# Performance work log

Hardware: AMD Instinct MI355X
Metric: run time of the kernel (lower is better)

The kernel has to match this reference:

```python
import jax, jax.numpy as jnp
import numpy as np

COMMITMENT_COST = 0.25


def setup_inputs() -> dict:
    key = jax.random.key(0)
    k1, k2 = jax.random.split(key)
    z = jax.random.normal(k1, (32, 256, 32, 32), dtype=jnp.float32)
    # Embedding init mirrors uniform(-1/codebook_size, 1/codebook_size)
    emb = jax.random.uniform(k2, (4096, 256), dtype=jnp.float32,
                             minval=-1.0 / 4096, maxval=1.0 / 4096)
    return {"z": z, "emb": emb}


def reference(z, emb):
    # z: [b, c, h, w] with c == token_size; emb: [codebook_size, token_size]
    b, c, h, w = z.shape
    z_bhwc = jnp.transpose(z, (0, 2, 3, 1))           # [b, h, w, c]
    z_flat = z_bhwc.reshape(-1, c)                    # [N, c]

    # Squared-distance matrix: ||z||^2 + ||e||^2 - 2 z e^T  -> [N, K]
    d = (jnp.sum(z_flat * z_flat, axis=1, keepdims=True)
         + jnp.sum(emb * emb, axis=1)
         - 2.0 * jnp.einsum('nd,kd->nk', z_flat, emb))

    idx = jnp.argmin(d, axis=1)                       # [N]
    z_q = emb[idx].reshape(z_bhwc.shape)              # [b, h, w, c]

    commitment_loss = COMMITMENT_COST * jnp.mean(
        (jax.lax.stop_gradient(z_q) - z_bhwc) ** 2)
    codebook_loss = jnp.mean((z_q - jax.lax.stop_gradient(z_bhwc)) ** 2)
    loss = commitment_loss + codebook_loss

    # Straight-through estimator
    z_q = z_bhwc + jax.lax.stop_gradient(z_q - z_bhwc)
    z_q = jnp.transpose(z_q, (0, 3, 1, 2))            # [b, c, h, w]

    min_encoding_indices = idx.reshape(b, h, w)
    return z_q, loss, commitment_loss, codebook_loss, min_encoding_indices
```

## Files before the change

### kernel.cpp

```cpp
#include <hip/hip_runtime.h>

#define CDIM 256
#define CB   4096
#define HW   1024
#define NTOK 32768
#define NELEM 8388608
#define MARGIN 3.5e-4f
#define OVCAP 64

typedef float f32x4 __attribute__((ext_vector_type(4)));
typedef short bf16x8 __attribute__((ext_vector_type(8)));
typedef unsigned int u32;
typedef unsigned long long u64;

__device__ __forceinline__ unsigned short f2bf(float x) {
    u32 b = __float_as_uint(x);
    return (unsigned short)((b + 0x7fffu + ((b >> 16) & 1u)) >> 16);
}
__device__ __forceinline__ u32 fenc(float f) {
    u32 b = __float_as_uint(f);
    return (b & 0x80000000u) ? ~b : (b | 0x80000000u);
}
__device__ __forceinline__ float fdec(u32 u) {
    return __uint_as_float((u & 0x80000000u) ? (u & 0x7fffffffu) : ~u);
}
__device__ __forceinline__ u64 shfl_xor_u64(u64 v, int s) {
    u32 lo = __shfl_xor((u32)v, s);
    u32 hi = __shfl_xor((u32)(v >> 32), s);
    return ((u64)hi << 32) | lo;
}
__device__ __forceinline__ void gl_lds16(const void* g, void* l) {
    __builtin_amdgcn_global_load_lds(
        (const __attribute__((address_space(1))) u32*)g,
        (__attribute__((address_space(3))) u32*)l, 16, 0, 0);
}


__global__ __launch_bounds__(1024) void prep(const float* __restrict__ z,
                                             const float* __restrict__ emb,
                                             float* __restrict__ zT,
                                             unsigned short* __restrict__ z_hip,
                                             float* __restrict__ zn,
                                             u32* __restrict__ ovcnt,
                                             float* __restrict__ enorm2,
                                             unsigned short* __restrict__ e_hip,
                                             u32* __restrict__ cnt2) {
    __shared__ float T[128][64];
    const int tid = threadIdx.x;
    const int tg = blockIdx.x;
    if (tid < 16) {
        const int code = tg * 8 + (tid >> 1);
        const int cl = code & 127;
        const int cgE = code >> 7;
        const int sxzE = (cl >> 1) & 3;
        float s = 0.f;
#pragma unroll
        for (int kb = 0; kb < 4; ++kb) {
            const int c0 = (tid & 1) * 128 + kb * 32;
            const int kc = c0 >> 5;
            __align__(16) unsigned short tmp[32];
#pragma unroll
            for (int q = 0; q < 8; ++q) {
                float4 v = *(const float4*)(emb + (size_t)code * CDIM + c0 + 4 * q);
                s += v.x * v.x + v.y * v.y + v.z * v.z + v.w * v.w;
                tmp[4 * q + 0] = f2bf(v.x); tmp[4 * q + 1] = f2bf(v.y);
                tmp[4 * q + 2] = f2bf(v.z); tmp[4 * q + 3] = f2bf(v.w);
            }
            uint4* dst4 = (uint4*)(e_hip + (((size_t)(cgE * 8 + kc) * 128 + cl) * 32));
#pragma unroll
            for (int q = 0; q < 4; ++q)
                dst4[q ^ sxzE] = *(uint4*)&tmp[8 * q];
        }
        s += __shfl_xor(s, 1);
        if ((tid & 1) == 0) enorm2[code] = s;
        if (tg == 0 && tid == 0) *cnt2 = 0u;
    }
    const int b = tg >> 4, hw0 = (tg * 64) & 1023;
    const float* zb = z + (size_t)b * (CDIM * HW) + hw0;
    const int tt = tid & 63;
    const int qrole = tid >> 6;
    const int kcl = qrole >> 2;
    const int qq = qrole & 3;
    const int gz = tg >> 1;
    const int rowl = (tg & 1) * 64 + tt;
    const int sxz = (tt >> 1) & 3;
    float zacc = 0.f;
#pragma unroll
    for (int grp = 0; grp < 2; ++grp) {
        const int c0 = grp * 128;
        __syncthreads();
#pragma unroll
        for (int p = 0; p < 8; ++p) {
            const int c = p * 16 + qrole;
            T[c][tt] = zb[(size_t)(c0 + c) * HW + tt];
        }
        __syncthreads();
        const int kc = grp * 4 + kcl;
        const int cb = kcl * 32 + qq * 8;
        float* dstT = zT + (size_t)(tg * 64 + tt) * CDIM + c0 + cb;
        __align__(16) unsigned short us[8];
#pragma unroll
        for (int q = 0; q < 2; ++q) {
            float4 v;
            v.x = T[cb + 4 * q + 0][tt]; v.y = T[cb + 4 * q + 1][tt];
            v.z = T[cb + 4 * q + 2][tt]; v.w = T[cb + 4 * q + 3][tt];
            ((float4*)dstT)[q] = v;
            zacc += v.x * v.x + v.y * v.y + v.z * v.z + v.w * v.w;
            us[4 * q + 0] = f2bf(v.x); us[4 * q + 1] = f2bf(v.y);
            us[4 * q + 2] = f2bf(v.z); us[4 * q + 3] = f2bf(v.w);
        }
        uint4* d4 = (uint4*)(z_hip + (((size_t)(gz * 8 + kc) * 128 + rowl) * 32));
        d4[qq ^ sxz] = *(uint4*)&us[0];
    }
    __syncthreads();
    float* zp = &T[0][0];
    zp[qrole * 64 + tt] = zacc;
    __syncthreads();
    if (tid < 64) {
        float s = 0.f;
#pragma unroll
        for (int r = 0; r < 16; ++r) s += zp[r * 64 + tid];
        zn[tg * 64 + tid] = s;
        ovcnt[tg * 64 + tid] = 0u;
    }
}


__global__ __launch_bounds__(256, 4) void p1(const unsigned short* __restrict__ z_hip,
                                             const unsigned short* __restrict__ e_hip,
                                             const float* __restrict__ enorm2,
                                             u64* __restrict__ cand,
                                             u32* __restrict__ ovcnt,
                                             u64* __restrict__ ovslot) {
    __shared__ __align__(16) unsigned short Bs[2][128 * 32];
    const int bid = blockIdx.x;
    const int xcd = bid & 7;
    const int seq = bid >> 3;
    const int rg = xcd * 32 + (seq >> 5);
    const int cg = seq & 31;
    const int tid = threadIdx.x;
    const int w = tid >> 6, lane = tid & 63;
    const int quad = lane >> 4, l15 = lane & 15;
    const int swz = (quad ^ ((l15 >> 1) & 3)) * 8;

    f32x4 acc[2][8];
#pragma unroll
    for (int i = 0; i < 2; ++i)
#pragma unroll
        for (int j = 0; j < 8; ++j)
#pragma unroll
            for (int e = 0; e < 4; ++e) acc[i][j][e] = 0.f;

    const char* gB = (const char*)e_hip + ((size_t)cg << 16) + w * 2048 + lane * 16;
    const char* gA0 = (const char*)z_hip + ((size_t)rg << 16)
                      + (w * 32 + l15) * 64 + swz * 2;
    char* lB = (char*)Bs + w * 2048;
    gl_lds16(gB, lB);           gl_lds16(gB + 1024, lB + 1024);
    gB += 8192;
    bf16x8 af0 = *(const bf16x8*)(gA0);
    bf16x8 af1 = *(const bf16x8*)(gA0 + 1024);
    __syncthreads();
#pragma unroll
    for (int kc = 0; kc < 8; ++kc) {
        const int cur = kc & 1;
        bf16x8 afn0, afn1;
        if (kc < 7) {
            char* dB = lB + (cur ^ 1) * 8192;
            gl_lds16(gB, dB);       gl_lds16(gB + 1024, dB + 1024);
            gB += 8192;
            asm volatile("" ::: "memory");
            const char* gA = gA0 + (size_t)(kc + 1) * 8192;
            afn0 = *(const bf16x8*)(gA);
            afn1 = *(const bf16x8*)(gA + 1024);
        }
        const unsigned short* B0 = Bs[cur];
        __builtin_amdgcn_s_setprio(1);
#pragma unroll
        for (int nh = 0; nh < 2; ++nh) {
            bf16x8 bfr[4];
#pragma unroll
            for (int nj = 0; nj < 4; ++nj)
                bfr[nj] = *(const bf16x8*)&B0[((nh * 4 + nj) * 16 + l15) * 32 + swz];
#pragma unroll
            for (int nj = 0; nj < 4; ++nj) {
                acc[0][nh * 4 + nj] = __builtin_amdgcn_mfma_f32_16x16x32_bf16(
                    af0, bfr[nj], acc[0][nh * 4 + nj], 0, 0, 0);
                acc[1][nh * 4 + nj] = __builtin_amdgcn_mfma_f32_16x16x32_bf16(
                    af1, bfr[nj], acc[1][nh * 4 + nj], 0, 0, 0);
            }
        }
        __builtin_amdgcn_s_setprio(0);
        if (kc < 7) {
            af0 = afn0; af1 = afn1;
            asm volatile("s_waitcnt vmcnt(2)" ::: "memory");
            __builtin_amdgcn_s_barrier();
            asm volatile("" ::: "memory");
        }
    }
    float en[8];
#pragma unroll
    for (int ni = 0; ni < 8; ++ni) en[ni] = enorm2[cg * 128 + ni * 16 + l15];
#pragma unroll
    for (int mi = 0; mi < 2; ++mi) {
#pragma unroll
        for (int r = 0; r < 4; ++r) {
            const int row = w * 32 + mi * 16 + quad * 4 + r;
            const int t = rg * 128 + row;
            float dv[8];
#pragma unroll
            for (int ni = 0; ni < 8; ++ni) dv[ni] = en[ni] - 2.0f * acc[mi][ni][r];
            float m = fminf(fminf(fminf(dv[0], dv[1]), fminf(dv[2], dv[3])),
                            fminf(fminf(dv[4], dv[5]), fminf(dv[6], dv[7])));
            m = fminf(m, __shfl_xor(m, 1));
            m = fminf(m, __shfl_xor(m, 2));
            m = fminf(m, __shfl_xor(m, 4));
            m = fminf(m, __shfl_xor(m, 8));
            u32 myni = 8u;
#pragma unroll
            for (int ni = 7; ni >= 0; --ni)
                if (dv[ni] == m) myni = (u32)ni;
            const unsigned long long bal = __ballot(myni < 8u);
            const int sl = __ffs((u32)((bal >> (quad << 4)) & 0xFFFFu)) - 1;
            if (l15 == sl) {
                const u32 k = (u32)(cg * 128 + (int)myni * 16 + l15);
                cand[((size_t)t << 5) + cg] = ((u64)fenc(m) << 32) | k;
            }
            const float thr = m + MARGIN;
#pragma unroll
            for (int ni = 0; ni < 8; ++ni) {
                if (dv[ni] <= thr && !(l15 == sl && ni == (int)myni)) {
                    const u32 k = (u32)(cg * 128 + ni * 16 + l15);
                    const u32 pos = atomicAdd(&ovcnt[t], 1u);
                    if (pos < (u32)OVCAP)
                        ovslot[(size_t)t * OVCAP + pos] = ((u64)fenc(dv[ni]) << 32) | k;
                }
            }
        }
    }
}

__global__ __launch_bounds__(256) void k5(const float* __restrict__ zT,
                                          const float* __restrict__ emb,
                                          const float* __restrict__ enorm2,
                                          const float* __restrict__ zn,
                                          const u64* __restrict__ cand,
                                          const u32* __restrict__ ovcnt,
                                          const u64* __restrict__ ovslot,
                                          float* __restrict__ idxf,
                                          float* __restrict__ dmin) {
    const int t = (blockIdx.x * 256 + threadIdx.x) >> 6;
    const int lane = threadIdx.x & 63;
    const u64 pkv = cand[((size_t)t << 5) + (lane & 31)];
    u64 g = pkv;
#pragma unroll
    for (int s = 1; s < 32; s <<= 1) {
        const u64 o = shfl_xor_u64(g, s);
        g = o < g ? o : g;
    }
    const float thr = fdec((u32)(g >> 32)) + MARGIN;
    const float4 za = ((const float4*)(zT + (size_t)t * CDIM))[lane];
    const float znv = zn[t];
    float bdv = 1e30f; int bk = 0x7fffffff;
    unsigned long long q = __ballot(fdec((u32)(pkv >> 32)) <= thr)
                           & 0xFFFFFFFFull;
    while (q) {
        const int i = __ffsll(q) - 1; q &= q - 1;
        const int k = __shfl((int)(u32)pkv, i);
        const float4 ea = ((const float4*)(emb + (size_t)k * CDIM))[lane];
        float p = za.x * ea.x + za.y * ea.y + za.z * ea.z + za.w * ea.w;
#pragma unroll
        for (int s = 1; s < 64; s <<= 1) p += __shfl_xor(p, s);
        const float t1 = znv + enorm2[k];
        const float d = t1 - 2.0f * p;
        if (d < bdv || (d == bdv && k < bk)) { bdv = d; bk = k; }
    }
    u32 n = ovcnt[t]; if (n > (u32)OVCAP) n = (u32)OVCAP;
    for (u32 i = 0; i < n; ++i) {
        const u64 ov = ovslot[(size_t)t * OVCAP + i];
        if (!(fdec((u32)(ov >> 32)) <= thr)) continue;
        const int k = (int)(u32)ov;
        const float4 ea = ((const float4*)(emb + (size_t)k * CDIM))[lane];
        float p = za.x * ea.x + za.y * ea.y + za.z * ea.z + za.w * ea.w;
#pragma unroll
        for (int s = 1; s < 64; s <<= 1) p += __shfl_xor(p, s);
        const float t1 = znv + enorm2[k];
        const float d = t1 - 2.0f * p;
        if (d < bdv || (d == bdv && k < bk)) { bdv = d; bk = k; }
    }
    if (lane == 0) {
        idxf[t] = (float)bk;
        dmin[t] = bdv;
    }
}

__global__ __launch_bounds__(1024) void k2(const float* __restrict__ emb,
                                           const float* __restrict__ idxf,
                                           const float* __restrict__ dmin,
                                           float* __restrict__ zq,
                                           float* __restrict__ out3,
                                           u32* __restrict__ cnt2) {
    __shared__ int ks[64];
    __shared__ float red[1024];
    __shared__ int lastFlag;
    const int tid = threadIdx.x;
    const int tok0 = blockIdx.x * 64;
    const int b = tok0 >> 10, hw0 = tok0 & 1023;
    if (tid < 64) ks[tid] = (int)idxf[tok0 + tid];
    __syncthreads();
    const int t4 = (tid & 15) * 4;
    const int ka = ks[t4], kb = ks[t4 + 1], kc = ks[t4 + 2], kd = ks[t4 + 3];
    float* outb = zq + (size_t)b * (CDIM * HW) + hw0 + t4;
    int c = tid >> 4;
#pragma unroll
    for (int p = 0; p < 4; ++p, c += 64) {
        float4 v;
        v.x = emb[(size_t)ka * CDIM + c];
        v.y = emb[(size_t)kb * CDIM + c];
        v.z = emb[(size_t)kc * CDIM + c];
        v.w = emb[(size_t)kd * CDIM + c];
        *(float4*)(outb + (size_t)c * HW) = v;
    }
    if (tid == 0) lastFlag = (atomicAdd(cnt2, 1u) == 511u) ? 1 : 0;
    __syncthreads();
    if (lastFlag) {
        const float4* d4 = (const float4*)dmin;
        float s = 0.f;
        for (int i = tid; i < NTOK / 4; i += 1024) {
            const float4 v = d4[i];
            s += (v.x + v.y) + (v.z + v.w);
        }
        red[tid] = s;
        __syncthreads();
        for (int o = 512; o > 0; o >>= 1) {
            if (tid < o) red[tid] += red[tid + o];
            __syncthreads();
        }
        if (tid == 0) {
            const float mse = red[0] / (float)NELEM;
            out3[0] = 1.25f * mse;
            out3[1] = 0.25f * mse;
            out3[2] = mse;
        }
    }
}

extern "C" void kernel_launch(void* const* d_in, const int* in_sizes, int n_in,
                              void* d_out, int out_size, void* d_ws, size_t ws_size,
                              hipStream_t stream) {
    const float* z   = (const float*)d_in[0];
    const float* emb = (const float*)d_in[1];
    float* out = (float*)d_out;
    char* w = (char*)d_ws;

    float* zn     = (float*)w;                       w += NTOK * 4;
    float* enorm2 = (float*)w;                       w += CB * 4;
    u32*   ovcnt  = (u32*)w;                         w += NTOK * 4;
    float* dmin   = (float*)w;                       w += NTOK * 4;
    u32*   cnt2   = (u32*)w;                         w += 256;
    float* zT     = (float*)w;                       w += (size_t)NTOK * CDIM * 4;
    unsigned short* z_hip = (unsigned short*)w;      w += (size_t)NTOK * CDIM * 2;
    unsigned short* e_hip = (unsigned short*)w;      w += (size_t)CB * CDIM * 2;
    u64*   cand   = (u64*)w;                         w += (size_t)NTOK * 32 * 8;
    u64*   ovslot = (u64*)w;                         w += (size_t)NTOK * OVCAP * 8;
    float* idxf = out + NELEM + 3;

    hipLaunchKernelGGL(prep, dim3(512),       dim3(1024), 0, stream,
                       z, emb, zT, z_hip, zn, ovcnt, enorm2, e_hip, cnt2);
    hipLaunchKernelGGL(p1,  dim3((NTOK / 128) * (CB / 128)), dim3(256), 0, stream,
                       z_hip, e_hip, enorm2, cand, ovcnt, ovslot);
    hipLaunchKernelGGL(k5,  dim3(NTOK / 4),   dim3(256), 0, stream,
                       zT, emb, enorm2, zn, cand, ovcnt, ovslot, idxf, dmin);
    hipLaunchKernelGGL(k2,  dim3(NTOK / 64),  dim3(1024), 0, stream,
                       emb, idxf, dmin, out, out + NELEM, cnt2);
}
```

Baseline: 262.2 us.

## Load codebook fragments directly from global memory instead of LDS double-buffering

```diff
diff --git a/kernel.cpp b/kernel.cpp
--- a/kernel.cpp
+++ b/kernel.cpp
@@ -28,11 +28,6 @@
     u32 lo = __shfl_xor((u32)v, s);
     u32 hi = __shfl_xor((u32)(v >> 32), s);
     return ((u64)hi << 32) | lo;
-}
-__device__ __forceinline__ void gl_lds16(const void* g, void* l) {
-    __builtin_amdgcn_global_load_lds(
-        (const __attribute__((address_space(1))) u32*)g,
-        (__attribute__((address_space(3))) u32*)l, 16, 0, 0);
 }
 
 
@@ -132,12 +127,8 @@
                                              u64* __restrict__ cand,
                                              u32* __restrict__ ovcnt,
                                              u64* __restrict__ ovslot) {
-    __shared__ __align__(16) unsigned short Bs[2][128 * 32];
     const int bid = blockIdx.x;
-    const int xcd = bid & 7;
-    const int seq = bid >> 3;
-    const int rg = xcd * 32 + (seq >> 5);
-    const int cg = seq & 31;
+    const int rg = bid >> 5, cg = bid & 31;
     const int tid = threadIdx.x;
     const int w = tid >> 6, lane = tid & 63;
     const int quad = lane >> 4, l15 = lane & 15;
@@ -151,36 +142,22 @@
 #pragma unroll
             for (int e = 0; e < 4; ++e) acc[i][j][e] = 0.f;
 
-    const char* gB = (const char*)e_hip + ((size_t)cg << 16) + w * 2048 + lane * 16;
     const char* gA0 = (const char*)z_hip + ((size_t)rg << 16)
                       + (w * 32 + l15) * 64 + swz * 2;
-    char* lB = (char*)Bs + w * 2048;
-    gl_lds16(gB, lB);           gl_lds16(gB + 1024, lB + 1024);
-    gB += 8192;
-    bf16x8 af0 = *(const bf16x8*)(gA0);
-    bf16x8 af1 = *(const bf16x8*)(gA0 + 1024);
-    __syncthreads();
+    const char* gB0 = (const char*)e_hip + ((size_t)cg << 16) + l15 * 64 + swz * 2;
+
 #pragma unroll
     for (int kc = 0; kc < 8; ++kc) {
-        const int cur = kc & 1;
-        bf16x8 afn0, afn1;
-        if (kc < 7) {
-            char* dB = lB + (cur ^ 1) * 8192;
-            gl_lds16(gB, dB);       gl_lds16(gB + 1024, dB + 1024);
-            gB += 8192;
-            asm volatile("" ::: "memory");
-            const char* gA = gA0 + (size_t)(kc + 1) * 8192;
-            afn0 = *(const bf16x8*)(gA);
-            afn1 = *(const bf16x8*)(gA + 1024);
-        }
-        const unsigned short* B0 = Bs[cur];
-        __builtin_amdgcn_s_setprio(1);
+        const char* gA = gA0 + kc * 8192;
+        const char* gB = gB0 + kc * 8192;
+        bf16x8 af0 = *(const bf16x8*)(gA);
+        bf16x8 af1 = *(const bf16x8*)(gA + 1024);
 #pragma unroll
         for (int nh = 0; nh < 2; ++nh) {
             bf16x8 bfr[4];
 #pragma unroll
             for (int nj = 0; nj < 4; ++nj)
-                bfr[nj] = *(const bf16x8*)&B0[((nh * 4 + nj) * 16 + l15) * 32 + swz];
+                bfr[nj] = *(const bf16x8*)(gB + (nh * 4 + nj) * 1024);
 #pragma unroll
             for (int nj = 0; nj < 4; ++nj) {
                 acc[0][nh * 4 + nj] = __builtin_amdgcn_mfma_f32_16x16x32_bf16(
@@ -188,13 +165,6 @@
                 acc[1][nh * 4 + nj] = __builtin_amdgcn_mfma_f32_16x16x32_bf16(
                     af1, bfr[nj], acc[1][nh * 4 + nj], 0, 0, 0);
             }
-        }
-        __builtin_amdgcn_s_setprio(0);
-        if (kc < 7) {
-            af0 = afn0; af1 = afn1;
-            asm volatile("s_waitcnt vmcnt(2)" ::: "memory");
-            __builtin_amdgcn_s_barrier();
-            asm volatile("" ::: "memory");
         }
     }
     float en[8];
```

After: 299.6 us. 1.14x slower.
